# Kernel optimization log

Hardware: AMD Instinct MI355X
Metric: run time of the kernel (lower is better)

## Reference

```python
import jax, jax.numpy as jnp
import numpy as np

TAU = 1.0
EPS_LN = 1e-5


def setup_inputs() -> dict:
    key = jax.random.key(0)
    ks = jax.random.split(key, 6)
    B, D, C, E, H = 32768, 768, 474, 3, 128
    x = jax.random.normal(ks[0], (B, D), dtype=jnp.float32)
    # pre-sampled uniform -> gumbel noise happens in reference; here store standard
    # gumbel noise directly (equivalent distribution to -log(-log(U)))
    u = jax.random.uniform(ks[1], (B, E), dtype=jnp.float32)
    gumbel_noise = -jnp.log(-jnp.log(u + 1e-20) + 1e-20)
    sel_w1 = jax.random.normal(ks[2], (D, H), dtype=jnp.float32) * (1.0 / np.sqrt(D))
    sel_b1 = jnp.zeros((H,), dtype=jnp.float32)
    sel_w2 = jax.random.normal(ks[3], (H, E), dtype=jnp.float32) * (1.0 / np.sqrt(H))
    sel_b2 = jnp.zeros((E,), dtype=jnp.float32)
    ln_gamma = jnp.ones((E, D), dtype=jnp.float32)
    ln_beta = jnp.zeros((E, D), dtype=jnp.float32)
    head_w = jax.random.normal(ks[4], (E, D, C), dtype=jnp.float32) * (1.0 / np.sqrt(D))
    head_b = jnp.zeros((E, C), dtype=jnp.float32)
    return {"x": x, "gumbel_noise": gumbel_noise, "sel_w1": sel_w1, "sel_b1": sel_b1,
            "sel_w2": sel_w2, "sel_b2": sel_b2, "ln_gamma": ln_gamma, "ln_beta": ln_beta,
            "head_w": head_w, "head_b": head_b}


def reference(x, gumbel_noise, sel_w1, sel_b1, sel_w2, sel_b2,
              ln_gamma, ln_beta, head_w, head_b):
    # selector MLP: Linear(768,128) -> ReLU -> Linear(128,3)
    h = jax.nn.relu(x @ sel_w1 + sel_b1)
    logits = h @ sel_w2 + sel_b2                       # [B, 3]

    # hard gumbel-softmax with straight-through estimator
    y = jax.nn.softmax((logits + gumbel_noise) / TAU, axis=-1)
    y_hard = jax.nn.one_hot(jnp.argmax(y, axis=-1), y.shape[-1], dtype=y.dtype)
    selection = jax.lax.stop_gradient(y_hard - y) + y  # [B, 3]

    # 3 expert heads: LayerNorm(768) -> Linear(768,474); dropout is identity (eval)
    mu = jnp.mean(x, axis=-1, keepdims=True)
    var = jnp.mean((x - mu) ** 2, axis=-1, keepdims=True)
    xn = (x - mu) * jax.lax.rsqrt(var + EPS_LN)        # [B, D]
    xs = xn[:, None, :] * ln_gamma[None] + ln_beta[None]   # [B, 3, D]
    outputs = jnp.einsum('bed,edc->bec', xs, head_w) + head_b  # [B, 3, C]

    # mask-and-sum combine
    return jnp.sum(outputs * selection[:, :, None], axis=1)    # [B, C]
```

## Files before the change

kernel.cpp:

```cpp
#include <hip/hip_runtime.h>
#include <hip/hip_bf16.h>
#include <math.h>

#define NB 32768
#define ND 768
#define NC 474
#define NCP 512
#define NE 3
#define NH 128
#define GAP_THR 0.035f
#define XB_OFF 4194304ull

typedef short v8s __attribute__((ext_vector_type(8)));
typedef float v4f __attribute__((ext_vector_type(4)));
typedef unsigned long long u64;

#define GLD16(gp, lp) __builtin_amdgcn_global_load_lds( \
    (const __attribute__((address_space(1))) void*)(gp), \
    (__attribute__((address_space(3))) void*)(lp), 16, 0, 0)

static __device__ __forceinline__ short f2bf(float f) {
    __hip_bfloat16 h = __float2bfloat16(f);
    return *reinterpret_cast<short*>(&h);
}

static __device__ __forceinline__ void vmwait(int n) {
    switch (n) {
    case 0:  asm volatile("s_waitcnt vmcnt(0)"  ::: "memory"); break;
    case 3:  asm volatile("s_waitcnt vmcnt(3)"  ::: "memory"); break;
    case 5:  asm volatile("s_waitcnt vmcnt(5)"  ::: "memory"); break;
    case 6:  asm volatile("s_waitcnt vmcnt(6)"  ::: "memory"); break;
    default: asm volatile("s_waitcnt vmcnt(10)" ::: "memory"); break;
    }
}

__global__ __launch_bounds__(256) void ln_convert(
    const float* __restrict__ x, float2* __restrict__ murs,
    short* __restrict__ xb)
{
    const int t = threadIdx.x;
    const int row = blockIdx.x * 16 + (t >> 4);
    const int q = t & 15;
    const float* xr = x + (size_t)row * ND;
    short* xo = xb + (size_t)row * ND;
    float4 v[12];
    #pragma unroll
    for (int i = 0; i < 12; ++i)
        v[i] = *(const float4*)(xr + (i * 16 + q) * 4);
    float s1 = 0.f, s2 = 0.f;
    #pragma unroll
    for (int i = 0; i < 12; ++i) {
        s1 += v[i].x + v[i].y + v[i].z + v[i].w;
        s2 += v[i].x*v[i].x + v[i].y*v[i].y + v[i].z*v[i].z + v[i].w*v[i].w;
    }
    #pragma unroll
    for (int i = 0; i < 12; ++i) {
        short4 o;
        o.x = f2bf(v[i].x); o.y = f2bf(v[i].y);
        o.z = f2bf(v[i].z); o.w = f2bf(v[i].w);
        *(short4*)(xo + (i * 16 + q) * 4) = o;
    }
    s1 += __shfl_xor(s1, 1); s2 += __shfl_xor(s2, 1);
    s1 += __shfl_xor(s1, 2); s2 += __shfl_xor(s2, 2);
    s1 += __shfl_xor(s1, 4); s2 += __shfl_xor(s2, 4);
    s1 += __shfl_xor(s1, 8); s2 += __shfl_xor(s2, 8);
    if (q == 0) {
        const float mu = s1 * (1.f / 768.f);
        const float var = s2 * (1.f / 768.f) - mu * mu;
        murs[row] = make_float2(mu, rsqrtf(var + 1e-5f));
    }
}

__global__ __launch_bounds__(256) void prep_kernel(
    const float* __restrict__ hw, const float* __restrict__ gamma,
    const float* __restrict__ beta, const float* __restrict__ w1,
    const float* __restrict__ hb,
    short* __restrict__ hwbT, short* __restrict__ w1bT,
    float* __restrict__ hbias, float* __restrict__ csumv)
{
    __shared__ float T[32][72];
    __shared__ float U[32][72];
    const int t = threadIdx.x;
    const int id = blockIdx.x;
    const float* src; short* dst; int stride, ncs; int e = 0, cc, kc;
    bool is_exp = (id < 576);
    if (is_exp) {
        e = id / 192; const int r2 = id % 192; cc = r2 / 24; kc = r2 % 24;
        src = hw + (size_t)e * ND * NC; stride = NC; ncs = NC;
        dst = hwbT + (size_t)e * NCP * ND;
    } else {
        const int j = id - 576; cc = j / 24; kc = j % 24;
        src = w1; stride = NH; ncs = NH; dst = w1bT;
    }
    const int c0 = cc * 64, k0 = kc * 32;
    {
        const int kl = t >> 3, c8 = (t & 7) * 8;
        const float g  = is_exp ? gamma[e * ND + k0 + kl] : 1.f;
        const float bb = is_exp ? beta[e * ND + k0 + kl]  : 0.f;
        #pragma unroll
        for (int j = 0; j < 8; ++j) {
            const int cg = c0 + c8 + j;
            const float v = (cg < ncs) ? src[(size_t)(k0 + kl) * stride + cg] : 0.f;
            T[kl][c8 + j] = v * g;
            U[kl][c8 + j] = v * bb;
        }
    }
    __syncthreads();
    {
        const int cl = t >> 2, q = t & 3;
        const int cg = c0 + cl;
        const int sp = q ^ ((cg >> 1) & 3);
        union { short s[8]; int4 v; } u;
        #pragma unroll
        for (int j = 0; j < 8; ++j) u.s[j] = f2bf(T[q * 8 + j][cl]);
        *(int4*)(dst + (size_t)cg * ND + k0 + sp * 8) = u.v;
    }
    if (is_exp && t < 64) {
        float sg = 0.f, sb = 0.f;
        #pragma unroll 8
        for (int k = 0; k < 32; ++k) {
            sg += T[k][t];
            sb += U[k][t];
        }
        const int c = c0 + t;
        if (kc == 0 && c < NC) sb += hb[e * NC + c];
        atomicAdd(&csumv[e * NCP + c], sg);
        atomicAdd(&hbias[e * NCP + c], sb);
    }
}

__global__ __launch_bounds__(256, 3) void selector_kernel(
    const short* __restrict__ xb, const float* __restrict__ gum,
    const short* __restrict__ w1bT, const float* __restrict__ b1,
    const float* __restrict__ w2, const float* __restrict__ b2,
    u64* __restrict__ counts,
    int* __restrict__ rowlist, int* __restrict__ redolist)
{
    __shared__ __align__(16) short As[4][2048];
    __shared__ __align__(16) short Bs[3][4096];
    __shared__ float wpart[4][64][3];
    __shared__ float b1s[NH], w2s[NH * 3];

    const int t = threadIdx.x;
    const int row0 = blockIdx.x * 64;
    const int w = t >> 6, l = t & 63;
    const int g = l >> 4, lm = l & 15;
    const int sr = t >> 2, sq = t & 3;

    if (t < NH) {
        b1s[t] = b1[t];
        w2s[t*3+0] = w2[t*3+0]; w2s[t*3+1] = w2[t*3+1]; w2s[t*3+2] = w2[t*3+2];
    }

    const int aslot = sq ^ ((sr >> 1) & 3);
    const short* axsrc = xb + (size_t)(row0 + sr) * ND + aslot * 8;
    const short* bsrc0 = w1bT + (size_t)(w * 32 +  0 + (l >> 2)) * ND + (l & 3) * 8;
    const short* bsrc1 = w1bT + (size_t)(w * 32 + 16 + (l >> 2)) * ND + (l & 3) * 8;
    const int aoff  = __builtin_amdgcn_readfirstlane(w * 512);
    const int boff0 = __builtin_amdgcn_readfirstlane((w * 32 +  0) * 32);
    const int boff1 = __builtin_amdgcn_readfirstlane((w * 32 + 16) * 32);

    v4f acc[4][2];
    #pragma unroll
    for (int i = 0; i < 4; ++i) { acc[i][0] = (v4f)(0.f); acc[i][1] = (v4f)(0.f); }

    __syncthreads();

    #pragma unroll
    for (int s = 0; s < 2; ++s) {
        GLD16(axsrc + s * 32, &As[s][0] + aoff);
        GLD16(bsrc0 + s * 32, &Bs[s][0] + boff0);
        GLD16(bsrc1 + s * 32, &Bs[s][0] + boff1);
    }

    #pragma unroll
    for (int ks = 0; ks < 24; ++ks) {
        const int curA = ks & 3;
        const int curB = ks % 3;
        if (ks < 22) {
            GLD16(axsrc + (ks + 2) * 32, &As[(ks + 2) & 3][0] + aoff);
            GLD16(bsrc0 + (ks + 2) * 32, &Bs[(ks + 2) % 3][0] + boff0);
            GLD16(bsrc1 + (ks + 2) * 32, &Bs[(ks + 2) % 3][0] + boff1);
            vmwait(6);
        } else {
            vmwait((23 - ks) * 3);
        }
        __builtin_amdgcn_sched_barrier(0);
        __builtin_amdgcn_s_barrier();

        v8s af[4];
        #pragma unroll
        for (int mf = 0; mf < 4; ++mf) {
            const int row = mf * 16 + lm;
            af[mf] = *(const v8s*)&As[curA][row * 32 + (g ^ ((lm >> 1) & 3)) * 8];
        }
        #pragma unroll
        for (int nf = 0; nf < 2; ++nf) {
            const int cl = w * 32 + nf * 16 + lm;
            const v8s bv = *(const v8s*)&Bs[curB][cl * 32 + (g ^ ((lm >> 1) & 3)) * 8];
            #pragma unroll
            for (int mf = 0; mf < 4; ++mf)
                acc[mf][nf] = __builtin_amdgcn_mfma_f32_16x16x32_bf16(
                    af[mf], bv, acc[mf][nf], 0, 0, 0);
        }
        asm volatile("s_waitcnt lgkmcnt(0)" ::: "memory");
        __builtin_amdgcn_sched_barrier(0);
    }

    #pragma unroll
    for (int mf = 0; mf < 4; ++mf) {
        float p[4][3] = {};
        #pragma unroll
        for (int nf = 0; nf < 2; ++nf) {
            const int cl = w * 32 + nf * 16 + lm;
            const float bb = b1s[cl];
            const float wa = w2s[cl*3], wb = w2s[cl*3+1], wc = w2s[cl*3+2];
            #pragma unroll
            for (int r = 0; r < 4; ++r) {
                const float h = fmaxf(acc[mf][nf][r] + bb, 0.f);
                p[r][0] = fmaf(h, wa, p[r][0]);
                p[r][1] = fmaf(h, wb, p[r][1]);
                p[r][2] = fmaf(h, wc, p[r][2]);
            }
        }
        #pragma unroll
        for (int m = 1; m < 16; m <<= 1)
            #pragma unroll
            for (int r = 0; r < 4; ++r) {
                p[r][0] += __shfl_xor(p[r][0], m);
                p[r][1] += __shfl_xor(p[r][1], m);
                p[r][2] += __shfl_xor(p[r][2], m);
            }
        if (lm == 0) {
            #pragma unroll
            for (int r = 0; r < 4; ++r) {
                const int row = mf * 16 + g * 4 + r;
                wpart[w][row][0] = p[r][0];
                wpart[w][row][1] = p[r][1];
                wpart[w][row][2] = p[r][2];
            }
        }
    }
    __syncthreads();

    if (t < 64) {
        const int grow = row0 + l;
        const float z0 = wpart[0][l][0] + wpart[1][l][0] + wpart[2][l][0]
                       + wpart[3][l][0] + b2[0] + gum[grow*3+0];
        const float z1 = wpart[0][l][1] + wpart[1][l][1] + wpart[2][l][1]
                       + wpart[3][l][1] + b2[1] + gum[grow*3+1];
        const float z2 = wpart[0][l][2] + wpart[1][l][2] + wpart[2][l][2]
                       + wpart[3][l][2] + b2[2] + gum[grow*3+2];
        int be = 0; float best = z0;
        if (z1 > best) { best = z1; be = 1; }
        if (z2 > best) { best = z2; be = 2; }
        const float second = (be==0) ? fmaxf(z1,z2) : (be==1) ? fmaxf(z0,z2) : fmaxf(z0,z1);
        if (best - second < GAP_THR) be = 3;

        const u64 m0 = __ballot(be == 0);
        const u64 m1 = __ballot(be == 1);
        const u64 m2 = __ballot(be == 2);
        const u64 m3 = __ballot(be == 3);
        u64 old = 0;
        if (l == 0) {
            const u64 add = (u64)__popcll(m0)
                          | ((u64)__popcll(m1) << 16)
                          | ((u64)__popcll(m2) << 32)
                          | ((u64)__popcll(m3) << 48);
            old = atomicAdd(counts, add);
        }
        const int blo = __shfl((int)(old & 0xFFFFFFFFull), 0);
        const int bhi = __shfl((int)(old >> 32), 0);
        old = ((u64)(unsigned)bhi << 32) | (u64)(unsigned)blo;
        const u64 mym = (be == 0) ? m0 : (be == 1) ? m1 : (be == 2) ? m2 : m3;
        const u64 below = (l == 63) ? 0x7FFFFFFFFFFFFFFFull : ((1ull << l) - 1ull);
        const int rank = __popcll(mym & below);
        const int base = (int)((old >> (16 * be)) & 0xFFFFull);
        const int idx = base + rank;
        if (be < 3) {
            if ((unsigned)idx < NB) rowlist[be * NB + idx] = grow;
        } else {
            if ((unsigned)idx < NB) redolist[idx] = grow;
        }
    }
}

__global__ __launch_bounds__(128) void redo_kernel(
    const float* __restrict__ x, const float* __restrict__ gum,
    const float* __restrict__ w1, const float* __restrict__ b1,
    const float* __restrict__ w2, const float* __restrict__ b2,
    u64* __restrict__ counts, int* __restrict__ rowlist,
    const int* __restrict__ redolist)
{
    const int t = threadIdx.x;
    int n = (int)((*counts >> 48) & 0xFFFFull);
    if (n > NB) n = NB;
    __shared__ float xs[ND];
    __shared__ double red[2][3];
    for (int i = blockIdx.x; i < n; i += gridDim.x) {
        const int row = redolist[i];
        {
            const float4* xp = (const float4*)(x + (size_t)row * ND);
            float4* xsv = (float4*)xs;
            xsv[t] = xp[t];
            if (t < 64) xsv[128 + t] = xp[128 + t];
        }
        __syncthreads();
        double h0 = 0.0, h1 = 0.0, h2 = 0.0, h3 = 0.0;
        double h4 = 0.0, h5 = 0.0, h6 = 0.0, h7 = 0.0;
        #pragma unroll 2
        for (int k = 0; k < ND; k += 8) {
            const float w0 = w1[(size_t)(k+0) * NH + t];
            const float w1v = w1[(size_t)(k+1) * NH + t];
            const float w2v = w1[(size_t)(k+2) * NH + t];
            const float w3 = w1[(size_t)(k+3) * NH + t];
            const float w4 = w1[(size_t)(k+4) * NH + t];
            const float w5 = w1[(size_t)(k+5) * NH + t];
            const float w6 = w1[(size_t)(k+6) * NH + t];
            const float w7 = w1[(size_t)(k+7) * NH + t];
            h0 = fma((double)xs[k+0], (double)w0, h0);
            h1 = fma((double)xs[k+1], (double)w1v, h1);
            h2 = fma((double)xs[k+2], (double)w2v, h2);
            h3 = fma((double)xs[k+3], (double)w3, h3);
            h4 = fma((double)xs[k+4], (double)w4, h4);
            h5 = fma((double)xs[k+5], (double)w5, h5);
            h6 = fma((double)xs[k+6], (double)w6, h6);
            h7 = fma((double)xs[k+7], (double)w7, h7);
        }
        double h = (((h0 + h1) + (h2 + h3)) + ((h4 + h5) + (h6 + h7)))
                 + (double)b1[t];
        h = h > 0.0 ? h : 0.0;
        double p0 = h * (double)w2[t * 3 + 0];
        double p1 = h * (double)w2[t * 3 + 1];
        double p2 = h * (double)w2[t * 3 + 2];
        #pragma unroll
        for (int m = 32; m >= 1; m >>= 1) {
            p0 += __shfl_xor(p0, m);
            p1 += __shfl_xor(p1, m);
            p2 += __shfl_xor(p2, m);
        }
        if ((t & 63) == 0) {
            red[t >> 6][0] = p0; red[t >> 6][1] = p1; red[t >> 6][2] = p2;
        }
        __syncthreads();
        if (t == 0) {
            double best = 0.0; int be = 0;
            #pragma unroll
            for (int e = 0; e < NE; ++e) {
                const double z = red[0][e] + red[1][e] + (double)b2[e]
                               + (double)gum[(size_t)row * 3 + e];
                if (e == 0 || z > best) { best = z; be = e; }
            }
            const u64 old = atomicAdd(counts, 1ull << (16 * be));
            const int pos = (int)((old >> (16 * be)) & 0xFFFFull);
            if ((unsigned)pos < NB) rowlist[be * NB + pos] = row;
        }
        __syncthreads();
    }
}

__global__ __launch_bounds__(256, 3) void head_kernel(
    const short* __restrict__ xb, const float2* __restrict__ murs,
    const short* __restrict__ hwbT, const float* __restrict__ hbias,
    const float* __restrict__ csumv,
    const u64* __restrict__ counts, const int* __restrict__ rowlist,
    float* __restrict__ out)
{
    const int e = blockIdx.z;
    int cnt = (int)((*counts >> (16 * e)) & 0xFFFFull);
    if (cnt > NB) cnt = NB;
    const int rc0 = blockIdx.y * 64;
    if (rc0 >= cnt) return;
    const int n0 = blockIdx.x * 256;

    __shared__ __align__(16) short As[4][2048];
    __shared__ __align__(16) short Bs[2][8192];
    __shared__ float hbs[256], css[256], rs_s[64], rm_s[64];
    __shared__ int rows_s[64];

    const int t = threadIdx.x;
    const int w = t >> 6, l = t & 63;
    const int g = l >> 4, lm = l & 15;
    const int sr = t >> 2, sq = t & 3;

    if (t < 64) {
        const int ri = rc0 + t;
        int rr = (ri < cnt) ? rowlist[e * NB + ri] : -1;
        if (rr >= NB) rr = -1;
        rows_s[t] = rr;
        const float2 mr = (rr >= 0) ? murs[rr] : make_float2(0.f, 0.f);
        rs_s[t] = mr.y;
        rm_s[t] = mr.y * mr.x;
    }
    hbs[t] = (n0 + t < NC) ? hbias[e * NCP + n0 + t] : 0.f;
    css[t] = (n0 + t < NC) ? csumv[e * NCP + n0 + t] : 0.f;

    const int ridx = rc0 + sr;
    int arow = (ridx < cnt) ? rowlist[e * NB + ridx] : 0;
    if ((unsigned)arow >= NB) arow = 0;
    const int aslot = sq ^ ((sr >> 1) & 3);
    const short* axsrc = xb + (size_t)arow * ND + aslot * 8;
    const short* hwe = hwbT + (size_t)e * NCP * ND + (size_t)n0 * ND;
    const int aoff = __builtin_amdgcn_readfirstlane(w * 512);

    v4f acc[4][4];
    #pragma unroll
    for (int i = 0; i < 4; ++i)
        #pragma unroll
        for (int j = 0; j < 4; ++j) acc[i][j] = (v4f)(0.f);

    #pragma unroll
    for (int i = 0; i < 4; ++i) {
        const int crow = w * 64 + i * 16 + (l >> 2);
        const int off = __builtin_amdgcn_readfirstlane((w * 64 + i * 16) * 32);
        GLD16(hwe + (size_t)crow * ND + (l & 3) * 8, &Bs[0][0] + off);
    }
    GLD16(axsrc,      &As[0][0] + aoff);
    GLD16(axsrc + 32, &As[1][0] + aoff);
    __syncthreads();

    #pragma unroll
    for (int ks = 0; ks < 24; ++ks) {
        const int curA = ks & 3;
        const int curB = ks & 1;
        if (ks < 23) {
            #pragma unroll
            for (int i = 0; i < 4; ++i) {
                const int crow = w * 64 + i * 16 + (l >> 2);
                const int off = __builtin_amdgcn_readfirstlane((w * 64 + i * 16) * 32);
                GLD16(hwe + (size_t)crow * ND + (ks + 1) * 32 + (l & 3) * 8,
                      &Bs[(ks + 1) & 1][0] + off);
            }
        }
        if (ks < 22) {
            GLD16(axsrc + (ks + 2) * 32, &As[(ks + 2) & 3][0] + aoff);
        }
        if (ks < 22)       vmwait(6);
        else if (ks == 22) vmwait(5);
        else               vmwait(0);
        __builtin_amdgcn_sched_barrier(0);
        __builtin_amdgcn_s_barrier();

        v8s af[4];
        #pragma unroll
        for (int mf = 0; mf < 4; ++mf) {
            const int row = mf * 16 + lm;
            af[mf] = *(const v8s*)&As[curA][row * 32 + (g ^ ((lm >> 1) & 3)) * 8];
        }
        #pragma unroll
        for (int nf = 0; nf < 4; ++nf) {
            const int cl = w * 64 + nf * 16 + lm;
            const v8s bv = *(const v8s*)&Bs[curB][cl * 32 + (g ^ ((lm >> 1) & 3)) * 8];
            #pragma unroll
            for (int mf = 0; mf < 4; ++mf)
                acc[mf][nf] = __builtin_amdgcn_mfma_f32_16x16x32_bf16(
                    af[mf], bv, acc[mf][nf], 0, 0, 0);
        }
        asm volatile("s_waitcnt lgkmcnt(0)" ::: "memory");
        __builtin_amdgcn_sched_barrier(0);
    }

    #pragma unroll
    for (int mf = 0; mf < 4; ++mf) {
        #pragma unroll
        for (int r = 0; r < 4; ++r) {
            const int rl = mf * 16 + g * 4 + r;
            const int orow = rows_s[rl];
            if (orow < 0) continue;
            const float rs = rs_s[rl], rm = rm_s[rl];
            float* op = out + (size_t)orow * NC;
            #pragma unroll
            for (int nf = 0; nf < 4; ++nf) {
                const int cl = w * 64 + nf * 16 + lm;
                const int c = n0 + cl;
                if (c < NC)
                    op[c] = acc[mf][nf][r] * rs - rm * css[cl] + hbs[cl];
            }
        }
    }
}

extern "C" void kernel_launch(void* const* d_in, const int* in_sizes, int n_in,
                              void* d_out, int out_size, void* d_ws, size_t ws_size,
                              hipStream_t stream) {
    const float* x     = (const float*)d_in[0];
    const float* gum   = (const float*)d_in[1];
    const float* w1    = (const float*)d_in[2];
    const float* b1    = (const float*)d_in[3];
    const float* w2    = (const float*)d_in[4];
    const float* b2    = (const float*)d_in[5];
    const float* gamma = (const float*)d_in[6];
    const float* beta  = (const float*)d_in[7];
    const float* hw    = (const float*)d_in[8];
    const float* hb    = (const float*)d_in[9];
    float* out = (float*)d_out;

    char* ws = (char*)d_ws;
    u64*    counts   = (u64*)ws;
    float2* murs     = (float2*)(ws + 256);
    int*    rowlist  = (int*)(ws + 262400);
    int*    redolist = (int*)(ws + 655616);
    float*  hbias    = (float*)(ws + 786688);
    float*  csumv    = (float*)(ws + 792832);
    short*  w1bT     = (short*)(ws + 798976);
    short*  hwbT     = (short*)(ws + 995584);
    short*  xbg      = (short*)(ws + XB_OFF);

    hipMemsetAsync(counts, 0, 16, stream);
    hipMemsetAsync(hbias, 0, 12288, stream);
    ln_convert<<<NB / 16, 256, 0, stream>>>(x, murs, xbg);
    prep_kernel<<<624, 256, 0, stream>>>(hw, gamma, beta, w1, hb,
                                         hwbT, w1bT, hbias, csumv);
    selector_kernel<<<NB / 64, 256, 0, stream>>>(xbg, gum, w1bT, b1, w2, b2,
                                                 counts, rowlist, redolist);
    redo_kernel<<<1024, 128, 0, stream>>>(x, gum, w1, b1, w2, b2,
                                          counts, rowlist, redolist);
    head_kernel<<<dim3(2, NB / 64, NE), 256, 0, stream>>>(
        xbg, murs, hwbT, hbias, csumv, counts, rowlist, out);
}
```

Measured before the change: 150.6 us.

## Deepen selector GEMM pipeline, double k-steps per barrier, fold memsets into kernel

Reworks the selector GEMM's load pipeline from 2-stage prefetch with 4/3 buffers to 4-stage prefetch with 8/6 buffers, processing two k-steps per barrier to halve synchronisation. LDS is unified into an 80KB union buffer reused for epilogue scratch, with launch bounds lowered to 2 blocks/CU. The two hipMemsetAsync calls are replaced by zeroing in block 0 of ln_convert, removing extra launches. Risks lower occupancy and a possible ordering hazard if prep_kernel atomics rely on the zeroing (same stream, so safe).

```diff
diff --git a/kernel.cpp b/kernel.cpp
--- a/kernel.cpp
+++ b/kernel.cpp
@@ -27,18 +27,24 @@
 static __device__ __forceinline__ void vmwait(int n) {
     switch (n) {
     case 0:  asm volatile("s_waitcnt vmcnt(0)"  ::: "memory"); break;
-    case 3:  asm volatile("s_waitcnt vmcnt(3)"  ::: "memory"); break;
     case 5:  asm volatile("s_waitcnt vmcnt(5)"  ::: "memory"); break;
     case 6:  asm volatile("s_waitcnt vmcnt(6)"  ::: "memory"); break;
+    case 12: asm volatile("s_waitcnt vmcnt(12)" ::: "memory"); break;
     default: asm volatile("s_waitcnt vmcnt(10)" ::: "memory"); break;
     }
 }
 
 __global__ __launch_bounds__(256) void ln_convert(
     const float* __restrict__ x, float2* __restrict__ murs,
-    short* __restrict__ xb)
+    short* __restrict__ xb, u64* __restrict__ counts,
+    float* __restrict__ hz )
 {
     const int t = threadIdx.x;
+    if (blockIdx.x == 0) {
+        if (t == 0) *counts = 0ull;
+        #pragma unroll
+        for (int i = 0; i < 12; ++i) hz[i * 256 + t] = 0.f;
+    }
     const int row = blockIdx.x * 16 + (t >> 4);
     const int q = t & 15;
     const float* xr = x + (size_t)row * ND;
@@ -129,28 +135,25 @@
     }
 }
 
-__global__ __launch_bounds__(256, 3) void selector_kernel(
+__global__ __launch_bounds__(256, 2) void selector_kernel(
     const short* __restrict__ xb, const float* __restrict__ gum,
     const short* __restrict__ w1bT, const float* __restrict__ b1,
     const float* __restrict__ w2, const float* __restrict__ b2,
     u64* __restrict__ counts,
     int* __restrict__ rowlist, int* __restrict__ redolist)
 {
-    __shared__ __align__(16) short As[4][2048];
-    __shared__ __align__(16) short Bs[3][4096];
-    __shared__ float wpart[4][64][3];
-    __shared__ float b1s[NH], w2s[NH * 3];
+    __shared__ __align__(16) char smem[81920];
+    short* As = (short*)smem;
+    short* Bs = (short*)(smem + 32768);
+    float* wpart = (float*)smem;
+    float* b1s   = (float*)(smem + 3072);
+    float* w2s   = (float*)(smem + 3584);
 
     const int t = threadIdx.x;
     const int row0 = blockIdx.x * 64;
     const int w = t >> 6, l = t & 63;
     const int g = l >> 4, lm = l & 15;
     const int sr = t >> 2, sq = t & 3;
-
-    if (t < NH) {
-        b1s[t] = b1[t];
-        w2s[t*3+0] = w2[t*3+0]; w2s[t*3+1] = w2[t*3+1]; w2s[t*3+2] = w2[t*3+2];
-    }
 
     const int aslot = sq ^ ((sr >> 1) & 3);
     const short* axsrc = xb + (size_t)(row0 + sr) * ND + aslot * 8;
@@ -164,48 +167,63 @@
     #pragma unroll
     for (int i = 0; i < 4; ++i) { acc[i][0] = (v4f)(0.f); acc[i][1] = (v4f)(0.f); }
 
-    __syncthreads();
-
-    #pragma unroll
-    for (int s = 0; s < 2; ++s) {
-        GLD16(axsrc + s * 32, &As[s][0] + aoff);
-        GLD16(bsrc0 + s * 32, &Bs[s][0] + boff0);
-        GLD16(bsrc1 + s * 32, &Bs[s][0] + boff1);
-    }
-
-    #pragma unroll
-    for (int ks = 0; ks < 24; ++ks) {
-        const int curA = ks & 3;
-        const int curB = ks % 3;
-        if (ks < 22) {
-            GLD16(axsrc + (ks + 2) * 32, &As[(ks + 2) & 3][0] + aoff);
-            GLD16(bsrc0 + (ks + 2) * 32, &Bs[(ks + 2) % 3][0] + boff0);
-            GLD16(bsrc1 + (ks + 2) * 32, &Bs[(ks + 2) % 3][0] + boff1);
+    #pragma unroll
+    for (int s = 0; s < 4; ++s) {
+        GLD16(axsrc + s * 32, As + s * 2048 + aoff);
+        GLD16(bsrc0 + s * 32, Bs + s * 4096 + boff0);
+        GLD16(bsrc1 + s * 32, Bs + s * 4096 + boff1);
+    }
+
+    #pragma unroll
+    for (int S = 0; S < 12; ++S) {
+        if (S <= 9) {
+            #pragma unroll
+            for (int u = 0; u < 2; ++u) {
+                const int j = 2 * S + 4 + u;
+                GLD16(axsrc + j * 32, As + (j & 7) * 2048 + aoff);
+                GLD16(bsrc0 + j * 32, Bs + (j % 6) * 4096 + boff0);
+                GLD16(bsrc1 + j * 32, Bs + (j % 6) * 4096 + boff1);
+            }
+            vmwait(12);
+        } else if (S == 10) {
             vmwait(6);
         } else {
-            vmwait((23 - ks) * 3);
+            vmwait(0);
         }
         __builtin_amdgcn_sched_barrier(0);
         __builtin_amdgcn_s_barrier();
 
-        v8s af[4];
-        #pragma unroll
-        for (int mf = 0; mf < 4; ++mf) {
-            const int row = mf * 16 + lm;
-            af[mf] = *(const v8s*)&As[curA][row * 32 + (g ^ ((lm >> 1) & 3)) * 8];
-        }
-        #pragma unroll
-        for (int nf = 0; nf < 2; ++nf) {
-            const int cl = w * 32 + nf * 16 + lm;
-            const v8s bv = *(const v8s*)&Bs[curB][cl * 32 + (g ^ ((lm >> 1) & 3)) * 8];
-            #pragma unroll
-            for (int mf = 0; mf < 4; ++mf)
-                acc[mf][nf] = __builtin_amdgcn_mfma_f32_16x16x32_bf16(
-                    af[mf], bv, acc[mf][nf], 0, 0, 0);
+        #pragma unroll
+        for (int u = 0; u < 2; ++u) {
+            const int j = 2 * S + u;
+            const short* Aj = As + (j & 7) * 2048;
+            const short* Bj = Bs + (j % 6) * 4096;
+            v8s af[4];
+            #pragma unroll
+            for (int mf = 0; mf < 4; ++mf) {
+                const int row = mf * 16 + lm;
+                af[mf] = *(const v8s*)&Aj[row * 32 + (g ^ ((lm >> 1) & 3)) * 8];
+            }
+            #pragma unroll
+            for (int nf = 0; nf < 2; ++nf) {
+                const int cl = w * 32 + nf * 16 + lm;
+                const v8s bv = *(const v8s*)&Bj[cl * 32 + (g ^ ((lm >> 1) & 3)) * 8];
+                #pragma unroll
+                for (int mf = 0; mf < 4; ++mf)
+                    acc[mf][nf] = __builtin_amdgcn_mfma_f32_16x16x32_bf16(
+                        af[mf], bv, acc[mf][nf], 0, 0, 0);
+            }
         }
         asm volatile("s_waitcnt lgkmcnt(0)" ::: "memory");
         __builtin_amdgcn_sched_barrier(0);
     }
+
+    __syncthreads();
+    if (t < NH) {
+        b1s[t] = b1[t];
+        w2s[t*3+0] = w2[t*3+0]; w2s[t*3+1] = w2[t*3+1]; w2s[t*3+2] = w2[t*3+2];
+    }
+    __syncthreads();
 
     #pragma unroll
     for (int mf = 0; mf < 4; ++mf) {
@@ -235,9 +253,9 @@
             #pragma unroll
             for (int r = 0; r < 4; ++r) {
                 const int row = mf * 16 + g * 4 + r;
-                wpart[w][row][0] = p[r][0];
-                wpart[w][row][1] = p[r][1];
-                wpart[w][row][2] = p[r][2];
+                wpart[(w * 64 + row) * 3 + 0] = p[r][0];
+                wpart[(w * 64 + row) * 3 + 1] = p[r][1];
+                wpart[(w * 64 + row) * 3 + 2] = p[r][2];
             }
         }
     }
@@ -245,12 +263,15 @@
 
     if (t < 64) {
         const int grow = row0 + l;
-        const float z0 = wpart[0][l][0] + wpart[1][l][0] + wpart[2][l][0]
-                       + wpart[3][l][0] + b2[0] + gum[grow*3+0];
-        const float z1 = wpart[0][l][1] + wpart[1][l][1] + wpart[2][l][1]
-                       + wpart[3][l][1] + b2[1] + gum[grow*3+1];
-        const float z2 = wpart[0][l][2] + wpart[1][l][2] + wpart[2][l][2]
-                       + wpart[3][l][2] + b2[2] + gum[grow*3+2];
+        const float z0 = wpart[(0*64+l)*3+0] + wpart[(1*64+l)*3+0]
+                       + wpart[(2*64+l)*3+0] + wpart[(3*64+l)*3+0]
+                       + b2[0] + gum[grow*3+0];
+        const float z1 = wpart[(0*64+l)*3+1] + wpart[(1*64+l)*3+1]
+                       + wpart[(2*64+l)*3+1] + wpart[(3*64+l)*3+1]
+                       + b2[1] + gum[grow*3+1];
+        const float z2 = wpart[(0*64+l)*3+2] + wpart[(1*64+l)*3+2]
+                       + wpart[(2*64+l)*3+2] + wpart[(3*64+l)*3+2]
+                       + b2[2] + gum[grow*3+2];
         int be = 0; float best = z0;
         if (z1 > best) { best = z1; be = 1; }
         if (z2 > best) { best = z2; be = 2; }
@@ -506,9 +527,7 @@
     short*  hwbT     = (short*)(ws + 995584);
     short*  xbg      = (short*)(ws + XB_OFF);
 
-    hipMemsetAsync(counts, 0, 16, stream);
-    hipMemsetAsync(hbias, 0, 12288, stream);
-    ln_convert<<<NB / 16, 256, 0, stream>>>(x, murs, xbg);
+    ln_convert<<<NB / 16, 256, 0, stream>>>(x, murs, xbg, counts, hbias);
     prep_kernel<<<624, 256, 0, stream>>>(hw, gamma, beta, w1, hb,
                                          hwbT, w1bT, hbias, csumv);
     selector_kernel<<<NB / 64, 256, 0, stream>>>(xbg, gum, w1bT, b1, w2, b2,
```

New measurement: 141.5 us. 6.1% less time.
